# Optimization experiments

Measured on AMD Instinct MI355X. Metric: run time of the kernel, lower is better.

Reference implementation:

```python
import jax, jax.numpy as jnp
import numpy as np

N = 50000
E = 800000
IN_C = 512
HID = 256
NUM_CLASS = (10, 25, 16, 350)


def _glorot(key, shape):
    fan_in, fan_out = shape[0], shape[1]
    lim = float(np.sqrt(6.0 / (fan_in + fan_out)))
    return jax.random.uniform(key, shape, jnp.float32, -lim, lim)


def setup_inputs() -> dict:
    key = jax.random.key(0)
    ks = jax.random.split(key, 16)
    x = jax.random.normal(ks[0], (N, IN_C), jnp.float32)
    edge_index = jax.random.randint(ks[1], (2, E), 0, N, jnp.int32)
    inp = {"x": x, "edge_index": edge_index}
    # gc1
    inp["W1"] = _glorot(ks[2], (IN_C, HID)); inp["b1"] = jnp.zeros((HID,), jnp.float32)
    # four GCNConv heads
    names = ["type", "school", "time", "author"]
    for i, (nm, nc) in enumerate(zip(names, NUM_CLASS)):
        inp[f"Wg_{nm}"] = _glorot(ks[3 + i], (HID, nc))
        inp[f"bg_{nm}"] = jnp.zeros((nc,), jnp.float32)
        inp[f"Wc_{nm}"] = _glorot(ks[7 + i], (nc, nc))
        inp[f"bc_{nm}"] = jnp.zeros((nc,), jnp.float32)
    return inp


def gcn_conv(x, W, b, src, dst, n):
    # GCNConv: out = D^{-1/2} (A + I) D^{-1/2} (x W) + b, symmetric norm.
    xw = x @ W  # [N, out]
    ones = jnp.ones((src.shape[0],), xw.dtype)
    deg = jax.ops.segment_sum(ones, dst, num_segments=n) + 1.0  # +1 from self-loop
    dinv = jax.lax.rsqrt(deg)
    norm = dinv[src] * dinv[dst]  # [E]
    agg = jax.ops.segment_sum(xw[src] * norm[:, None], dst, num_segments=n)
    # self-loop contribution: norm_ii = dinv_i^2
    return agg + xw * (dinv * dinv)[:, None] + b


def reference(x, edge_index, W1, b1,
              Wg_type, bg_type, Wc_type, bc_type,
              Wg_school, bg_school, Wc_school, bc_school,
              Wg_time, bg_time, Wc_time, bc_time,
              Wg_author, bg_author, Wc_author, bc_author):
    src, dst = edge_index[0], edge_index[1]
    n = x.shape[0]
    h = jax.nn.relu(gcn_conv(x, W1, b1, src, dst, n))  # dropout is identity in eval

    def head(Wg, bg, Wc, bc):
        g = gcn_conv(h, Wg, bg, src, dst, n)
        return jax.nn.softmax(g @ Wc + bc, axis=-1)

    out_type = head(Wg_type, bg_type, Wc_type, bc_type)
    out_school = head(Wg_school, bg_school, Wc_school, bc_school)
    out_time = head(Wg_time, bg_time, Wc_time, bc_time)
    out_author = head(Wg_author, bg_author, Wc_author, bc_author)
    return (out_type, out_school, out_time, out_author)
```

## Files before the change

kernel.cpp:

```cpp
#include <hip/hip_runtime.h>
#include <hip/hip_bf16.h>
#include <cstdint>
#include <cstddef>
#include <math.h>

#define NN 50000
#define NE 800000
#define INC 512
#define HIDC 256
#define NBLK ((NN + 255) / 256)

typedef __attribute__((ext_vector_type(8))) short s8v;
typedef __attribute__((ext_vector_type(4))) float f4v;
typedef unsigned int u32;

#define VMC(n)  asm volatile("s_waitcnt vmcnt(" #n ")" ::: "memory")
#define LGKM0   asm volatile("s_waitcnt lgkmcnt(0)" ::: "memory")
#define BAR()   do { __builtin_amdgcn_s_barrier(); asm volatile("" ::: "memory"); } while (0)

__device__ __forceinline__ float b2f(unsigned short u) {
    return __uint_as_float(((unsigned)u) << 16);
}
__device__ __forceinline__ unsigned short f2b(float f) {
    __hip_bfloat16 h = __float2bfloat16(f);
    return *reinterpret_cast<unsigned short*>(&h);
}
__device__ __forceinline__ void gload16(const void* g, void* l) {
    __builtin_amdgcn_global_load_lds(
        (const __attribute__((address_space(1))) u32*)g,
        (__attribute__((address_space(3))) u32*)l, 16, 0, 0);
}

__global__ void k_deg_count(const int* __restrict__ dst, int* __restrict__ cnt, int e) {
    int i = blockIdx.x * 256 + threadIdx.x;
    if (i < e) atomicAdd(&cnt[dst[i]], 1);
}
__global__ void k_scan1(const int* __restrict__ cnt, int* __restrict__ excl,
                        int* __restrict__ bsum, float* __restrict__ dinv, int n) {
    __shared__ int s[256];
    int i = blockIdx.x * 256 + threadIdx.x;
    int v = (i < n) ? cnt[i] : 0;
    if (i < n) dinv[i] = rsqrtf((float)v + 1.0f);
    s[threadIdx.x] = v;
    __syncthreads();
    for (int off = 1; off < 256; off <<= 1) {
        int t = (threadIdx.x >= off) ? s[threadIdx.x - off] : 0;
        __syncthreads();
        s[threadIdx.x] += t;
        __syncthreads();
    }
    if (i < n) excl[i] = s[threadIdx.x] - v;
    if (threadIdx.x == 255) bsum[blockIdx.x] = s[255];
}
__global__ void k_scan2(int* __restrict__ bsum, int* __restrict__ bsumx, int nb) {
    __shared__ int s[256];
    int t = threadIdx.x;
    int v = (t < nb) ? bsum[t] : 0;
    s[t] = v;
    __syncthreads();
    for (int off = 1; off < 256; off <<= 1) {
        int tt = (t >= off) ? s[t - off] : 0;
        __syncthreads();
        s[t] += tt;
        __syncthreads();
    }
    if (t < nb) bsumx[t] = s[t] - v;
}
__global__ void k_scan3(int* __restrict__ rowptr, const int* __restrict__ bsumx, int n, int e) {
    int i = blockIdx.x * 256 + threadIdx.x;
    if (i < n) rowptr[i] += bsumx[blockIdx.x];
    if (i == 0) rowptr[n] = e;
}
__global__ void k_fill(const int* __restrict__ src, const int* __restrict__ dst,
                       const int* __restrict__ rowptr, int* __restrict__ cursor,
                       int* __restrict__ col, int e) {
    int i = blockIdx.x * 256 + threadIdx.x;
    if (i >= e) return;
    int d = dst[i];
    int pos = rowptr[d] + atomicAdd(&cursor[d], 1);
    col[pos] = src[i];
}

__global__ void k_tr2(const float* __restrict__ Wg3, const float* __restrict__ Wc3,
                      float* __restrict__ Wg3t, float* __restrict__ Wc3t) {
    int t = blockIdx.x * 256 + threadIdx.x;
    if (t < 256 * 350) { int k = t / 350, i = t - k * 350; Wg3t[i * 256 + k] = Wg3[t]; }
    if (t < 350 * 350) { int i = t / 350, j = t - i * 350; Wc3t[j * 350 + i] = Wc3[t]; }
}

__global__ void k_prep(const float* __restrict__ W1,
                       const float* __restrict__ Wg0, const float* __restrict__ Wc0,
                       const float* __restrict__ bg0, const float* __restrict__ bc0,
                       const float* __restrict__ Wg1, const float* __restrict__ Wc1,
                       const float* __restrict__ bg1, const float* __restrict__ bc1,
                       const float* __restrict__ Wg2, const float* __restrict__ Wc2,
                       const float* __restrict__ bg2, const float* __restrict__ bc2,
                       const float* __restrict__ Wg3, const float* __restrict__ Wc3,
                       const float* __restrict__ bg3, const float* __restrict__ bc3,
                       const float* __restrict__ Wg3t, const float* __restrict__ Wc3t,
                       unsigned short* __restrict__ W1t_sw, unsigned short* __restrict__ Wftp,
                       float* __restrict__ bfv)
{
    __shared__ float Wcj[352];
    int b = blockIdx.x, tid = threadIdx.x;
    if (b < 512) {
        int t = b * 256 + tid;
        int c = t >> 9, k = t & 511;
        int chs = ((k >> 3) & 7) ^ (c & 7);
        W1t_sw[(size_t)(k >> 6) * 16384 + c * 64 + chs * 8 + (k & 7)] = f2b(W1[(size_t)k * 256 + c]);
    } else if (b < 960) {
        int j = b - 512, k = tid;
        float s = 0.f;
        if (j < 350) {
            for (int i = tid; i < 350; i += 256) Wcj[i] = Wc3t[(size_t)j * 350 + i];
            __syncthreads();
            for (int i = 0; i < 350; ++i) s += Wg3t[i * 256 + k] * Wcj[i];
        } else if (j >= 352 && j < 362) {
            int jj = j - 352; for (int i = 0; i < 10; ++i) s += Wg0[k * 10 + i] * Wc0[i * 10 + jj];
        } else if (j >= 362 && j < 387) {
            int jj = j - 362; for (int i = 0; i < 25; ++i) s += Wg1[k * 25 + i] * Wc1[i * 25 + jj];
        } else if (j >= 387 && j < 403) {
            int jj = j - 387; for (int i = 0; i < 16; ++i) s += Wg2[k * 16 + i] * Wc2[i * 16 + jj];
        }
        Wftp[((size_t)(k >> 5) * 448 + j) * 32 + (k & 31)] = f2b(s);
    } else {
        int j = (b - 960) * 256 + tid;
        if (j >= 448) return;
        float s = 0.f;
        if (j < 350)                  { s = bc3[j]; for (int i = 0; i < 350; ++i) s += bg3[i] * Wc3[(size_t)i * 350 + j]; }
        else if (j >= 352 && j < 362) { int jj = j - 352; s = bc0[jj]; for (int i = 0; i < 10; ++i) s += bg0[i] * Wc0[i * 10 + jj]; }
        else if (j >= 362 && j < 387) { int jj = j - 362; s = bc1[jj]; for (int i = 0; i < 25; ++i) s += bg1[i] * Wc1[i * 25 + jj]; }
        else if (j >= 387 && j < 403) { int jj = j - 387; s = bc2[jj]; for (int i = 0; i < 16; ++i) s += bg2[i] * Wc2[i * 16 + jj]; }
        bfv[j] = s;
    }
}

__global__ __launch_bounds__(256, 2) void gemm1_conv(
    const float* __restrict__ X, const unsigned short* __restrict__ Bsw,
    unsigned short* __restrict__ C, int M)
{
    __shared__ s8v lds[5120];
    const int t = threadIdx.x;
    const int lane = t & 63, wv = t >> 6;
    const int wvM = wv >> 1, wvN = wv & 1;
    const int l15 = lane & 15, lq = lane >> 4;
    const int row0 = blockIdx.x * 64;

    const int arow = t >> 2, q = t & 3;
    int gr = row0 + arow; if (gr >= M) gr = M - 1;
    const float* asrc = X + (size_t)gr * INC + q * 16;
    const int awp0 = arow * 8 + ((q * 2) ^ (arow & 7));
    const int awp1 = arow * 8 + ((q * 2 + 1) ^ (arow & 7));

    float4 fa0, fa1, fa2, fa3;
#define STAGE_B1(kbn, buf) do { \
    const unsigned short* bs_ = Bsw + (size_t)(kbn) * 2048 * 8; \
    int bb_ = 1024 + (buf) * 2048; \
    _Pragma("unroll") \
    for (int sB = 0; sB < 8; ++sB) { \
        int g_ = (wv * 8 + sB) * 64; \
        gload16(bs_ + (size_t)(g_ + lane) * 8, (void*)&lds[bb_ + g_]); \
    } } while (0)
#define LOAD_A1(kbn) do { \
    fa0 = *(const float4*)(asrc + (kbn) * 64); \
    fa1 = *(const float4*)(asrc + (kbn) * 64 + 4); \
    fa2 = *(const float4*)(asrc + (kbn) * 64 + 8); \
    fa3 = *(const float4*)(asrc + (kbn) * 64 + 12); } while (0)

    f4v acc[2][8] = {};
    STAGE_B1(0, 0);
    LOAD_A1(0);
    for (int kb = 0; kb < 8; ++kb) {
        const int cur = kb & 1, nxt = cur ^ 1;
        if (kb < 7) STAGE_B1(kb + 1, nxt);
        if (kb < 7) { VMC(8); } else { VMC(0); }
        s8v o0, o1;
        o0[0]=(short)f2b(fa0.x); o0[1]=(short)f2b(fa0.y); o0[2]=(short)f2b(fa0.z); o0[3]=(short)f2b(fa0.w);
        o0[4]=(short)f2b(fa1.x); o0[5]=(short)f2b(fa1.y); o0[6]=(short)f2b(fa1.z); o0[7]=(short)f2b(fa1.w);
        o1[0]=(short)f2b(fa2.x); o1[1]=(short)f2b(fa2.y); o1[2]=(short)f2b(fa2.z); o1[3]=(short)f2b(fa2.w);
        o1[4]=(short)f2b(fa3.x); o1[5]=(short)f2b(fa3.y); o1[6]=(short)f2b(fa3.z); o1[7]=(short)f2b(fa3.w);
        lds[cur * 512 + awp0] = o0;
        lds[cur * 512 + awp1] = o1;
        if (kb < 7) LOAD_A1(kb + 1);
        LGKM0; BAR();
        const int ab = cur * 512, bb = 1024 + cur * 2048;
#pragma unroll
        for (int kk = 0; kk < 2; ++kk) {
            const int chr = (kk * 4 + lq) ^ (l15 & 7);
            s8v a0 = lds[ab + (wvM * 32 + l15) * 8 + chr];
            s8v a1 = lds[ab + (wvM * 32 + 16 + l15) * 8 + chr];
#pragma unroll
            for (int cf = 0; cf < 8; ++cf) {
                s8v bf = lds[bb + (wvN * 128 + cf * 16 + l15) * 8 + chr];
                acc[0][cf] = __builtin_amdgcn_mfma_f32_16x16x32_bf16(a0, bf, acc[0][cf], 0, 0, 0);
                acc[1][cf] = __builtin_amdgcn_mfma_f32_16x16x32_bf16(a1, bf, acc[1][cf], 0, 0, 0);
            }
        }
        LGKM0; BAR();
    }
#pragma unroll
    for (int rf = 0; rf < 2; ++rf)
#pragma unroll
    for (int r = 0; r < 4; ++r) {
        int row = row0 + wvM * 32 + rf * 16 + lq * 4 + r;
        if (row >= M) continue;
#pragma unroll
        for (int cf = 0; cf < 8; ++cf)
            C[(size_t)row * HIDC + wvN * 128 + cf * 16 + l15] = f2b(acc[rf][cf][r]);
    }
#undef STAGE_B1
#undef LOAD_A1
}

template <bool RELU, bool BIAS>
__global__ __launch_bounds__(256) void k_gather2(
    const unsigned short* __restrict__ feat, const int* __restrict__ rowptr,
    const int* __restrict__ col, const float* __restrict__ dinv,
    const float* __restrict__ bias, unsigned short* __restrict__ out, int n)
{
    int unit = (blockIdx.x * 256 + threadIdx.x) >> 5;
    int l32 = threadIdx.x & 31;
    if (unit >= n) return;
    float di = dinv[unit];
    int p0 = rowptr[unit], p1 = rowptr[unit + 1];
    int deg = p1 - p0;
    int myc = 0; float mydj = 0.f;
    if (l32 < deg) { myc = col[p0 + l32]; mydj = dinv[myc]; }
    float acc[8] = {};
    int dmin = deg < 32 ? deg : 32;
    int base = threadIdx.x & 32;
#pragma unroll 2
    for (int q = 0; q < dmin; ++q) {
        int j = __shfl(myc, base + q);
        float dj = __shfl(mydj, base + q);
        s8v v = *(const s8v*)(feat + (size_t)j * HIDC + l32 * 8);
#pragma unroll
        for (int c = 0; c < 8; ++c) acc[c] += dj * b2f((unsigned short)v[c]);
    }
    for (int p = p0 + 32; p < p1; ++p) {
        int j = col[p];
        float dj = dinv[j];
        s8v v = *(const s8v*)(feat + (size_t)j * HIDC + l32 * 8);
#pragma unroll
        for (int c = 0; c < 8; ++c) acc[c] += dj * b2f((unsigned short)v[c]);
    }
    s8v sv = *(const s8v*)(feat + (size_t)unit * HIDC + l32 * 8);
    float dd = di * di;
    s8v o;
#pragma unroll
    for (int c = 0; c < 8; ++c) {
        float r = di * acc[c] + dd * b2f((unsigned short)sv[c]);
        if (BIAS) r += bias[l32 * 8 + c];
        if (RELU) r = fmaxf(r, 0.f);
        o[c] = (short)f2b(r);
    }
    *(s8v*)(out + (size_t)unit * HIDC + l32 * 8) = o;
}

__global__ __launch_bounds__(512, 4) void gemm2_heads(
    const unsigned short* __restrict__ Ap, const unsigned short* __restrict__ Bp,
    const float* __restrict__ bfv,
    float* __restrict__ o0, float* __restrict__ o1,
    float* __restrict__ o2, float* __restrict__ o3, int M)
{
    __shared__ s8v lds[4096];
    const int t = threadIdx.x;
    const int lane = t & 63, wv = t >> 6;
    const int wvM = wv >> 2, wvN = wv & 3;
    const int l15 = lane & 15, lq = lane >> 4;
    const int row0 = blockIdx.x * 64;

#define STAGE2(kbn, buf) do { \
    if (wv == 0) { \
        _Pragma("unroll") \
        for (int s = 0; s < 4; ++s) { \
            int ci_ = s * 64 + lane; \
            int row_ = ci_ >> 2, ch_ = ci_ & 3; \
            int grow_ = row0 + row_; if (grow_ >= M) grow_ = M - 1; \
            gload16(Ap + (size_t)grow_ * HIDC + (kbn) * 32 + ch_ * 8, \
                    (void*)&lds[(buf) * 256 + s * 64]); \
        } \
    } else { \
        _Pragma("unroll") \
        for (int s = 0; s < 4; ++s) { \
            int bg_ = (wv - 1) * 4 + s; \
            int bci_ = bg_ * 64 + lane; \
            int j_ = bci_ >> 2, ch_ = bci_ & 3; \
            gload16(Bp + ((size_t)(kbn) * 448 + j_) * 32 + ch_ * 8, \
                    (void*)&lds[512 + (buf) * 1792 + bg_ * 64]); \
        } \
    } } while (0)

    f4v acc[2][7] = {};
    STAGE2(0, 0);
    for (int kb = 0; kb < 8; ++kb) {
        const int cur = kb & 1, nxt = cur ^ 1;
        if (kb < 7) STAGE2(kb + 1, nxt);
        if (kb < 7) { VMC(4); } else { VMC(0); }
        LGKM0; BAR();
        const int ab = cur * 256, bb = 512 + cur * 1792;
        s8v a0 = lds[ab + (wvM * 32 + l15) * 4 + lq];
        s8v a1 = lds[ab + (wvM * 32 + 16 + l15) * 4 + lq];
#pragma unroll
        for (int cf = 0; cf < 7; ++cf) {
            s8v bf = lds[bb + (wvN * 112 + cf * 16 + l15) * 4 + lq];
            acc[0][cf] = __builtin_amdgcn_mfma_f32_16x16x32_bf16(a0, bf, acc[0][cf], 0, 0, 0);
            acc[1][cf] = __builtin_amdgcn_mfma_f32_16x16x32_bf16(a1, bf, acc[1][cf], 0, 0, 0);
        }
        LGKM0; BAR();
    }
#undef STAGE2
    float* smx = (float*)lds;
#pragma unroll
    for (int cf = 0; cf < 7; ++cf) {
        float bb = bfv[wvN * 112 + cf * 16 + l15];
#pragma unroll
        for (int rf = 0; rf < 2; ++rf)
#pragma unroll
        for (int r = 0; r < 4; ++r) acc[rf][cf][r] += bb;
    }
#pragma unroll
    for (int rf = 0; rf < 2; ++rf)
#pragma unroll
    for (int r = 0; r < 4; ++r) {
        float ma = -1e30f, m1 = -1e30f, m2 = -1e30f, m3 = -1e30f;
#pragma unroll
        for (int cf = 0; cf < 7; ++cf) {
            int colc = wvN * 112 + cf * 16 + l15;
            float v = acc[rf][cf][r];
            if (colc < 350) ma = fmaxf(ma, v);
            else if (colc >= 352 && colc < 362) m1 = fmaxf(m1, v);
            else if (colc >= 362 && colc < 387) m2 = fmaxf(m2, v);
            else if (colc >= 387 && colc < 403) m3 = fmaxf(m3, v);
        }
#pragma unroll
        for (int o = 8; o; o >>= 1) {
            ma = fmaxf(ma, __shfl_xor(ma, o));
            m1 = fmaxf(m1, __shfl_xor(m1, o));
            m2 = fmaxf(m2, __shfl_xor(m2, o));
            m3 = fmaxf(m3, __shfl_xor(m3, o));
        }
        int rowl = wvM * 32 + rf * 16 + lq * 4 + r;
        if (l15 == 0) {
            smx[rowl * 4 + wvN] = ma;
            if (wvN == 3) {
                smx[512 + rowl * 3 + 0] = m1;
                smx[512 + rowl * 3 + 1] = m2;
                smx[512 + rowl * 3 + 2] = m3;
            }
        }
    }
    __syncthreads();
#pragma unroll
    for (int rf = 0; rf < 2; ++rf)
#pragma unroll
    for (int r = 0; r < 4; ++r) {
        int rowl = wvM * 32 + rf * 16 + lq * 4 + r;
        float am = fmaxf(fmaxf(smx[rowl * 4 + 0], smx[rowl * 4 + 1]),
                         fmaxf(smx[rowl * 4 + 2], smx[rowl * 4 + 3]));
        float m1 = 0.f, m2 = 0.f, m3 = 0.f;
        if (wvN == 3) {
            m1 = smx[512 + rowl * 3 + 0];
            m2 = smx[512 + rowl * 3 + 1];
            m3 = smx[512 + rowl * 3 + 2];
        }
        float sa = 0.f, s1 = 0.f, s2 = 0.f, s3 = 0.f;
#pragma unroll
        for (int cf = 0; cf < 7; ++cf) {
            int colc = wvN * 112 + cf * 16 + l15;
            float v = acc[rf][cf][r];
            float e = 0.f;
            if (colc < 350)                     { e = __expf(v - am); sa += e; }
            else if (colc >= 352 && colc < 362) { e = __expf(v - m1); s1 += e; }
            else if (colc >= 362 && colc < 387) { e = __expf(v - m2); s2 += e; }
            else if (colc >= 387 && colc < 403) { e = __expf(v - m3); s3 += e; }
            acc[rf][cf][r] = e;
        }
#pragma unroll
        for (int o = 8; o; o >>= 1) {
            sa += __shfl_xor(sa, o); s1 += __shfl_xor(s1, o);
            s2 += __shfl_xor(s2, o); s3 += __shfl_xor(s3, o);
        }
        if (l15 == 0) {
            smx[256 + rowl * 4 + wvN] = sa;
            if (wvN == 3) {
                smx[704 + rowl * 3 + 0] = s1;
                smx[704 + rowl * 3 + 1] = s2;
                smx[704 + rowl * 3 + 2] = s3;
            }
        }
    }
    __syncthreads();
#pragma unroll
    for (int rf = 0; rf < 2; ++rf)
#pragma unroll
    for (int r = 0; r < 4; ++r) {
        int rowl = wvM * 32 + rf * 16 + lq * 4 + r;
        int row = row0 + rowl;
        if (row >= M) continue;
        float ia = 1.f / (smx[256 + rowl * 4 + 0] + smx[256 + rowl * 4 + 1] +
                          smx[256 + rowl * 4 + 2] + smx[256 + rowl * 4 + 3]);
        float i1 = 0.f, i2 = 0.f, i3 = 0.f;
        if (wvN == 3) {
            i1 = 1.f / smx[704 + rowl * 3 + 0];
            i2 = 1.f / smx[704 + rowl * 3 + 1];
            i3 = 1.f / smx[704 + rowl * 3 + 2];
        }
#pragma unroll
        for (int cf = 0; cf < 7; ++cf) {
            int colc = wvN * 112 + cf * 16 + l15;
            float e = acc[rf][cf][r];
            if (colc < 350)                     o3[(size_t)row * 350 + colc]        = e * ia;
            else if (colc >= 352 && colc < 362) o0[(size_t)row * 10 + (colc - 352)] = e * i1;
            else if (colc >= 362 && colc < 387) o1[(size_t)row * 25 + (colc - 362)] = e * i2;
            else if (colc >= 387 && colc < 403) o2[(size_t)row * 16 + (colc - 387)] = e * i3;
        }
    }
}

extern "C" void kernel_launch(void* const* d_in, const int* in_sizes, int n_in,
                              void* d_out, int out_size, void* d_ws, size_t ws_size,
                              hipStream_t stream)
{
    const float* x   = (const float*)d_in[0];
    const int*   ei  = (const int*)d_in[1];
    const float* W1  = (const float*)d_in[2];
    const float* b1  = (const float*)d_in[3];
    const float* Wg0 = (const float*)d_in[4];
    const float* bg0 = (const float*)d_in[5];
    const float* Wc0 = (const float*)d_in[6];
    const float* bc0 = (const float*)d_in[7];
    const float* Wg1 = (const float*)d_in[8];
    const float* bg1 = (const float*)d_in[9];
    const float* Wc1 = (const float*)d_in[10];
    const float* bc1 = (const float*)d_in[11];
    const float* Wg2 = (const float*)d_in[12];
    const float* bg2 = (const float*)d_in[13];
    const float* Wc2 = (const float*)d_in[14];
    const float* bc2 = (const float*)d_in[15];
    const float* Wg3 = (const float*)d_in[16];
    const float* bg3 = (const float*)d_in[17];
    const float* Wc3 = (const float*)d_in[18];
    const float* bc3 = (const float*)d_in[19];
    const int* srcI = ei;
    const int* dstI = ei + NE;

    char* ws = (char*)d_ws;
    size_t off = 0;
    auto alloc = [&](size_t bytes) { void* p = ws + off; off += (bytes + 255) & ~(size_t)255; return p; };
    float* dinv   = (float*)alloc(50176 * 4);
    int*   rowptr = (int*)  alloc(50432 * 4);
    int*   cnt    = (int*)  alloc(2 * 50176 * 4);
    int*   cursor = cnt + 50176;
    int*   bsum   = (int*)  alloc(1024);
    int*   bsumx  = (int*)  alloc(1024);
    int*   col    = (int*)  alloc((size_t)NE * 4);
    unsigned short* W1t_sw = (unsigned short*)alloc(256 * 512 * 2);
    unsigned short* Wftp   = (unsigned short*)alloc(448 * 256 * 2);
    float* bfv   = (float*)alloc(448 * 4);
    float* Wg3t  = (float*)alloc(350 * 256 * 4);
    float* Wc3t  = (float*)alloc(350 * 350 * 4);
    unsigned short* xwb = (unsigned short*)alloc((size_t)NN * HIDC * 2);
    unsigned short* hb  = (unsigned short*)alloc((size_t)NN * HIDC * 2);
    unsigned short* ahb = xwb;

    float* out0 = (float*)d_out;
    float* out1 = out0 + (size_t)NN * 10;
    float* out2 = out1 + (size_t)NN * 25;
    float* out3 = out2 + (size_t)NN * 16;

    hipMemsetAsync(cnt, 0, 2 * 50176 * 4, stream);
    k_deg_count<<<(NE + 255) / 256, 256, 0, stream>>>(dstI, cnt, NE);
    k_scan1<<<NBLK, 256, 0, stream>>>(cnt, rowptr, bsum, dinv, NN);
    k_scan2<<<1, 256, 0, stream>>>(bsum, bsumx, NBLK);
    k_scan3<<<NBLK, 256, 0, stream>>>(rowptr, bsumx, NN, NE);
    k_fill<<<(NE + 255) / 256, 256, 0, stream>>>(srcI, dstI, rowptr, cursor, col, NE);

    k_tr2<<<(350 * 350 + 255) / 256, 256, 0, stream>>>(Wg3, Wc3, Wg3t, Wc3t);
    k_prep<<<962, 256, 0, stream>>>(W1,
                                    Wg0, Wc0, bg0, bc0, Wg1, Wc1, bg1, bc1,
                                    Wg2, Wc2, bg2, bc2, Wg3, Wc3, bg3, bc3,
                                    Wg3t, Wc3t, W1t_sw, Wftp, bfv);

    gemm1_conv<<<(NN + 63) / 64, 256, 0, stream>>>(x, W1t_sw, xwb, NN);
    k_gather2<true, true><<<(NN + 7) / 8, 256, 0, stream>>>(xwb, rowptr, col, dinv, b1, hb, NN);
    k_gather2<false, false><<<(NN + 7) / 8, 256, 0, stream>>>(hb, rowptr, col, dinv, nullptr, ahb, NN);
    gemm2_heads<<<(NN + 63) / 64, 512, 0, stream>>>(ahb, Wftp, bfv, out0, out1, out2, out3, NN);
}
```

Measured before the change: 360.2 us.

## Swizzle gemm2 LDS layout, preload B fragments, and raise MFMA wave priority

Rewrites the packed head-weight layout and the gemm2 staging addresses so that LDS tiles are stored chunk-major with an XOR swizzle. The goal is to avoid bank conflicts on fragment reads. gemm2 now reads all B fragments into registers before a barrier and then runs the MFMAs, which replaces the trailing barrier with a mid-iteration one. Both GEMMs raise wave priority around the MFMA loop. Reading everything before the barrier costs extra registers, and the barrier placement has to stay correct for double-buffer reuse.

```diff
diff --git a/kernel.cpp b/kernel.cpp
--- a/kernel.cpp
+++ b/kernel.cpp
@@ -16,6 +16,7 @@
 
 #define VMC(n)  asm volatile("s_waitcnt vmcnt(" #n ")" ::: "memory")
 #define LGKM0   asm volatile("s_waitcnt lgkmcnt(0)" ::: "memory")
+#define SCHED0  __builtin_amdgcn_sched_barrier(0)
 #define BAR()   do { __builtin_amdgcn_s_barrier(); asm volatile("" ::: "memory"); } while (0)
 
 __device__ __forceinline__ float b2f(unsigned short u) {
@@ -122,7 +123,8 @@
         } else if (j >= 387 && j < 403) {
             int jj = j - 387; for (int i = 0; i < 16; ++i) s += Wg2[k * 16 + i] * Wc2[i * 16 + jj];
         }
-        Wftp[((size_t)(k >> 5) * 448 + j) * 32 + (k & 31)] = f2b(s);
+        int kb = k >> 5, ch = (k >> 3) & 3, e = k & 7;
+        Wftp[(((size_t)kb * 4 + ch) * 448 + (j ^ (ch * 2))) * 8 + e] = f2b(s);
     } else {
         int j = (b - 960) * 256 + tid;
         if (j >= 448) return;
@@ -184,6 +186,7 @@
         if (kb < 7) LOAD_A1(kb + 1);
         LGKM0; BAR();
         const int ab = cur * 512, bb = 1024 + cur * 2048;
+        __builtin_amdgcn_s_setprio(1);
 #pragma unroll
         for (int kk = 0; kk < 2; ++kk) {
             const int chr = (kk * 4 + lq) ^ (l15 & 7);
@@ -196,6 +199,7 @@
                 acc[1][cf] = __builtin_amdgcn_mfma_f32_16x16x32_bf16(a1, bf, acc[1][cf], 0, 0, 0);
             }
         }
+        __builtin_amdgcn_s_setprio(0);
         LGKM0; BAR();
     }
 #pragma unroll
@@ -274,19 +278,15 @@
     if (wv == 0) { \
         _Pragma("unroll") \
         for (int s = 0; s < 4; ++s) { \
-            int ci_ = s * 64 + lane; \
-            int row_ = ci_ >> 2, ch_ = ci_ & 3; \
-            int grow_ = row0 + row_; if (grow_ >= M) grow_ = M - 1; \
-            gload16(Ap + (size_t)grow_ * HIDC + (kbn) * 32 + ch_ * 8, \
+            int grow_ = row0 + (lane ^ (s * 2)); if (grow_ >= M) grow_ = M - 1; \
+            gload16(Ap + (size_t)grow_ * HIDC + (kbn) * 32 + s * 8, \
                     (void*)&lds[(buf) * 256 + s * 64]); \
         } \
     } else { \
         _Pragma("unroll") \
         for (int s = 0; s < 4; ++s) { \
             int bg_ = (wv - 1) * 4 + s; \
-            int bci_ = bg_ * 64 + lane; \
-            int j_ = bci_ >> 2, ch_ = bci_ & 3; \
-            gload16(Bp + ((size_t)(kbn) * 448 + j_) * 32 + ch_ * 8, \
+            gload16(Bp + ((size_t)(kbn) * 1792 + bg_ * 64 + lane) * 8, \
                     (void*)&lds[512 + (buf) * 1792 + bg_ * 64]); \
         } \
     } } while (0)
@@ -297,17 +297,24 @@
         const int cur = kb & 1, nxt = cur ^ 1;
         if (kb < 7) STAGE2(kb + 1, nxt);
         if (kb < 7) { VMC(4); } else { VMC(0); }
-        LGKM0; BAR();
+        BAR();
         const int ab = cur * 256, bb = 512 + cur * 1792;
-        s8v a0 = lds[ab + (wvM * 32 + l15) * 4 + lq];
-        s8v a1 = lds[ab + (wvM * 32 + 16 + l15) * 4 + lq];
+        const int l15x = l15 ^ (lq * 2);
+        s8v a0 = lds[ab + lq * 64 + wvM * 32 + l15x];
+        s8v a1 = lds[ab + lq * 64 + wvM * 32 + 16 + l15x];
+        s8v bfr[7];
+#pragma unroll
+        for (int cf = 0; cf < 7; ++cf)
+            bfr[cf] = lds[bb + lq * 448 + wvN * 112 + cf * 16 + l15x];
+        LGKM0; SCHED0;
+        BAR();
+        __builtin_amdgcn_s_setprio(1);
 #pragma unroll
         for (int cf = 0; cf < 7; ++cf) {
-            s8v bf = lds[bb + (wvN * 112 + cf * 16 + l15) * 4 + lq];
-            acc[0][cf] = __builtin_amdgcn_mfma_f32_16x16x32_bf16(a0, bf, acc[0][cf], 0, 0, 0);
-            acc[1][cf] = __builtin_amdgcn_mfma_f32_16x16x32_bf16(a1, bf, acc[1][cf], 0, 0, 0);
-        }
-        LGKM0; BAR();
+            acc[0][cf] = __builtin_amdgcn_mfma_f32_16x16x32_bf16(a0, bfr[cf], acc[0][cf], 0, 0, 0);
+            acc[1][cf] = __builtin_amdgcn_mfma_f32_16x16x32_bf16(a1, bfr[cf], acc[1][cf], 0, 0, 0);
+        }
+        __builtin_amdgcn_s_setprio(0);
     }
 #undef STAGE2
     float* smx = (float*)lds;
```

Measured after the change: 345.3 us. -4.2%, faster.
